# Performance work log

Measured on AMD Instinct MI355X. Metric: run time of the kernel, lower is better.

The kernel has to match this reference:

```python
import jax, jax.numpy as jnp
import numpy as np

HID, NH, NKV, HD = 2048, 16, 8, 128
EPS = 1e-6
THETA = 10000.0
SCALE = HD ** -0.5


def setup_inputs() -> dict:
    key = jax.random.key(0)
    ks = jax.random.split(key, 6)
    S = 2048
    return {
        "positions": jnp.arange(S, dtype=jnp.int32),
        "hidden_states": jax.random.normal(ks[0], (S, HID), dtype=jnp.float32),
        "layernorm_weight": jax.random.uniform(ks[1], (HID,), dtype=jnp.float32, minval=0.5, maxval=1.5),
        "w_qkv": jax.random.normal(ks[2], ((NH + 2 * NKV) * HD, HID), dtype=jnp.float32) * 0.02,
        "w_o": jax.random.normal(ks[3], (HID, NH * HD), dtype=jnp.float32) * 0.02,
        "q_norm_w": jax.random.uniform(ks[4], (HD,), dtype=jnp.float32, minval=0.5, maxval=1.5),
        "k_norm_w": jax.random.uniform(ks[5], (HD,), dtype=jnp.float32, minval=0.5, maxval=1.5),
    }


def _rmsnorm(x, w, eps=EPS):
    var = jnp.mean(jnp.square(x), axis=-1, keepdims=True)
    return x * jax.lax.rsqrt(var + eps) * w


def _rope(x, cos, sin):
    # x: [S, h, HD]; cos/sin: [S, 1, HD//2] (neox-style rotate-half)
    x1, x2 = x[..., : HD // 2], x[..., HD // 2 :]
    return jnp.concatenate([x1 * cos - x2 * sin, x2 * cos + x1 * sin], axis=-1)


def reference(positions, hidden_states, layernorm_weight, w_qkv, w_o, q_norm_w, k_norm_w):
    S = hidden_states.shape[0]
    # Fused RMSNorm + QKV projection
    hn = _rmsnorm(hidden_states, layernorm_weight)
    qkv = hn @ w_qkv.T  # [S, (NH+2*NKV)*HD]
    q, k, v = jnp.split(qkv, [NH * HD, (NH + NKV) * HD], axis=-1)
    q = q.reshape(S, NH, HD)
    k = k.reshape(S, NKV, HD)
    v = v.reshape(S, NKV, HD)
    # Per-head QK RMSNorm
    q = _rmsnorm(q, q_norm_w)
    k = _rmsnorm(k, k_norm_w)
    # RoPE
    inv_freq = 1.0 / (THETA ** (jnp.arange(0, HD, 2, dtype=jnp.float32) / HD))
    freqs = positions.astype(jnp.float32)[:, None] * inv_freq  # [S, HD//2]
    cos = jnp.cos(freqs)[:, None, :]
    sin = jnp.sin(freqs)[:, None, :]
    q = _rope(q, cos, sin)
    k = _rope(k, cos, sin)
    # GQA: expand kv heads to match query heads
    rep = NH // NKV
    k = jnp.repeat(k, rep, axis=1)  # [S, NH, HD]
    v = jnp.repeat(v, rep, axis=1)
    # Causal attention
    scores = jnp.einsum("shd,thd->hst", q, k) * SCALE  # [NH, S, S]
    causal = jnp.tril(jnp.ones((S, S), dtype=bool))
    scores = jnp.where(causal, scores, jnp.finfo(scores.dtype).min)
    probs = jax.nn.softmax(scores, axis=-1)
    out = jnp.einsum("hst,thd->shd", probs, v)  # [S, NH, HD]
    # Output projection
    return out.reshape(S, NH * HD) @ w_o.T
```

## Files before the change

kernel.cpp:

```cpp
#include <hip/hip_runtime.h>
#include <hip/hip_bf16.h>
#include <math.h>

#define HID 2048
#define NH 16
#define NKV 8
#define HD 128
#define SEQ 2048
#define EPS 1e-6f
#define SCALE 0.08838834764831845f

typedef __attribute__((ext_vector_type(8))) short bf8_t;
typedef __attribute__((ext_vector_type(4))) float f4_t;

__device__ __forceinline__ short f2bf(float f) {
    union { __hip_bfloat16 h; short s; } u;
    u.h = __float2bfloat16(f);
    return u.s;
}
__device__ __forceinline__ float bf2f(short s) {
    union { short s; __hip_bfloat16 h; } u;
    u.s = s;
    return __bfloat162float(u.h);
}
__device__ __forceinline__ bf8_t pack8(const float4& a, const float4& b) {
    bf8_t r;
    r[0] = f2bf(a.x); r[1] = f2bf(a.y); r[2] = f2bf(a.z); r[3] = f2bf(a.w);
    r[4] = f2bf(b.x); r[5] = f2bf(b.y); r[6] = f2bf(b.z); r[7] = f2bf(b.w);
    return r;
}
__device__ __forceinline__ void gload16(const short* g, short* l) {
    __builtin_amdgcn_global_load_lds(
        (const __attribute__((address_space(1))) unsigned int*)g,
        (__attribute__((address_space(3))) unsigned int*)l, 16, 0, 0);
}

__device__ __forceinline__ float wave_reduce_sum(float v) {
#pragma unroll
    for (int off = 32; off > 0; off >>= 1) v += __shfl_xor(v, off);
    return v;
}

__global__ __launch_bounds__(256) void prep_kernel(
    const float* __restrict__ w_qkv, short* __restrict__ wqb,
    const float* __restrict__ w_o, short* __restrict__ wob,
    const float* __restrict__ x, const float* __restrict__ w,
    short* __restrict__ out) {
    int bid = blockIdx.x;
    int tid = threadIdx.x;
    if (bid < 4096) {
        int i = bid * 256 + tid;
        float4 a = *(const float4*)(w_qkv + (size_t)i * 8);
        float4 b = *(const float4*)(w_qkv + (size_t)i * 8 + 4);
        *(bf8_t*)(wqb + (size_t)i * 8) = pack8(a, b);
        return;
    }
    if (bid < 6144) {
        int i = (bid - 4096) * 256 + tid;
        float4 a = *(const float4*)(w_o + (size_t)i * 8);
        float4 b = *(const float4*)(w_o + (size_t)i * 8 + 4);
        *(bf8_t*)(wob + (size_t)i * 8) = pack8(a, b);
        return;
    }
    int row = bid - 6144;
    const float* xr = x + (size_t)row * HID;
    float4 a = *(const float4*)(xr + tid * 8);
    float4 b = *(const float4*)(xr + tid * 8 + 4);
    float ss = a.x * a.x + a.y * a.y + a.z * a.z + a.w * a.w +
               b.x * b.x + b.y * b.y + b.z * b.z + b.w * b.w;
    ss = wave_reduce_sum(ss);
    __shared__ float part[4];
    __shared__ float s_scale;
    if ((tid & 63) == 0) part[tid >> 6] = ss;
    __syncthreads();
    if (tid == 0) {
        float t = part[0] + part[1] + part[2] + part[3];
        s_scale = rsqrtf(t / (float)HID + EPS);
    }
    __syncthreads();
    float sc = s_scale;
    float4 wa = *(const float4*)(w + tid * 8);
    float4 wb = *(const float4*)(w + tid * 8 + 4);
    float4 oa = make_float4(a.x * sc * wa.x, a.y * sc * wa.y,
                            a.z * sc * wa.z, a.w * sc * wa.w);
    float4 ob = make_float4(b.x * sc * wb.x, b.y * sc * wb.y,
                            b.z * sc * wb.z, b.w * sc * wb.w);
    *(bf8_t*)(out + (size_t)row * HID + tid * 8) = pack8(oa, ob);
}

template <int MODE>
__global__ __launch_bounds__(256) void gemm_mfma_kernel(
    const short* __restrict__ A, const short* __restrict__ B,
    float* __restrict__ Cf, short* __restrict__ Q, short* __restrict__ Kp,
    short* __restrict__ Vr, int M, int N, int K) {
    __shared__ short As[128][64];
    __shared__ short Bs[128][64];
    int tid = threadIdx.x;
    int wv = tid >> 6, lane = tid & 63;
    int n16 = lane & 15, qd = lane >> 4;
    int m0 = blockIdx.y * 128, n0 = blockIdx.x * 128;
    int wm = (wv >> 1) * 64, wn = (wv & 1) * 64;
    int sr8 = lane >> 3, slot = lane & 7;

    size_t ainv[4], binv[4];
#pragma unroll
    for (int it = 0; it < 4; ++it) {
        int row = wv * 32 + it * 8 + sr8;
        int chunk = (slot - row) & 7;
        ainv[it] = (size_t)(m0 + row) * K + chunk * 8;
        binv[it] = (size_t)(n0 + row) * K + chunk * 8;
    }

    f4_t acc[4][4];
#pragma unroll
    for (int i = 0; i < 4; ++i)
#pragma unroll
        for (int j = 0; j < 4; ++j) acc[i][j] = (f4_t){0.f, 0.f, 0.f, 0.f};

    for (int k0 = 0; k0 < K; k0 += 64) {
        __syncthreads();
#pragma unroll
        for (int it = 0; it < 4; ++it) {
            gload16(A + ainv[it] + k0, &As[wv * 32 + it * 8][0]);
            gload16(B + binv[it] + k0, &Bs[wv * 32 + it * 8][0]);
        }
        __syncthreads();

        bf8_t af[4][2], bf[4][2];
#pragma unroll
        for (int t = 0; t < 4; ++t)
#pragma unroll
            for (int ks = 0; ks < 2; ++ks) {
                int ar = wm + t * 16 + n16;
                af[t][ks] = *(const bf8_t*)&As[ar][(((ks * 4 + qd) + ar) & 7) * 8];
                int br = wn + t * 16 + n16;
                bf[t][ks] = *(const bf8_t*)&Bs[br][(((ks * 4 + qd) + br) & 7) * 8];
            }
#pragma unroll
        for (int ks = 0; ks < 2; ++ks)
#pragma unroll
            for (int mt = 0; mt < 4; ++mt)
#pragma unroll
                for (int nt = 0; nt < 4; ++nt)
                    acc[mt][nt] = __builtin_amdgcn_mfma_f32_16x16x32_bf16(
                        af[mt][ks], bf[nt][ks], acc[mt][nt], 0, 0, 0);
    }

#pragma unroll
    for (int mt = 0; mt < 4; ++mt)
#pragma unroll
        for (int nt = 0; nt < 4; ++nt)
#pragma unroll
            for (int r = 0; r < 4; ++r) {
                int gm = m0 + wm + mt * 16 + qd * 4 + r;
                int gn = n0 + wn + nt * 16 + n16;
                float v = acc[mt][nt][r];
                if (MODE == 0) {
                    Cf[(size_t)gm * N + gn] = v;
                } else {
                    if (gn < NH * HD)
                        Q[(size_t)gm * (NH * HD) + gn] = f2bf(v);
                    else if (gn < (NH + NKV) * HD)
                        Kp[(size_t)gm * (NKV * HD) + (gn - NH * HD)] = f2bf(v);
                    else
                        Vr[(size_t)gm * (NKV * HD) + (gn - (NH + NKV) * HD)] = f2bf(v);
                }
            }
}

__global__ __launch_bounds__(256) void mid_kernel(
    const short* __restrict__ vr, short* __restrict__ vt,
    short* __restrict__ q, short* __restrict__ k,
    const float* __restrict__ qw, const float* __restrict__ kw,
    const int* __restrict__ pos) {
    int bid = blockIdx.x;
    int tid = threadIdx.x;
    if (bid < 512) {
        __shared__ short t[64][64];
        int s0 = (bid & 31) * 64, d0 = (bid >> 5) * 64;
        int sl = tid >> 3, ch = tid & 7;
#pragma unroll
        for (int it = 0; it < 2; ++it) {
            int s_local = it * 32 + sl;
            bf8_t vv = *(const bf8_t*)(vr + (size_t)(s0 + s_local) * (NKV * HD) + d0 + ch * 8);
            *(bf8_t*)&t[s_local][((ch + s_local) & 7) * 8] = vv;
        }
        __syncthreads();
#pragma unroll
        for (int it = 0; it < 2; ++it) {
            int d_local = it * 32 + sl;
            int sbase = ch * 8;
            bf8_t o;
#pragma unroll
            for (int j = 0; j < 8; ++j) {
                int s = sbase + j;
                o[j] = t[s][(((d_local >> 3) + s) & 7) * 8 + (d_local & 7)];
            }
            *(bf8_t*)(vt + (size_t)(d0 + d_local) * SEQ + s0 + sbase) = o;
        }
        return;
    }
    int u = (bid - 512) * 2 + (tid >> 7);
    int ui = tid >> 7, d = tid & 127;
    int s = u / 24, hh = u % 24;
    short* ptr;
    const float* w;
    if (hh < NH) {
        ptr = q + (size_t)s * (NH * HD) + hh * HD;
        w = qw;
    } else {
        ptr = k + (size_t)s * (NKV * HD) + (hh - NH) * HD;
        w = kw;
    }
    float x = bf2f(ptr[d]);
    float ss = wave_reduce_sum(x * x);
    __shared__ float part[2][2];
    if ((d & 63) == 0) part[ui][d >> 6] = ss;
    __syncthreads();
    float tot = part[ui][0] + part[ui][1];
    float xn = x * rsqrtf(tot / (float)HD + EPS) * w[d];
    __shared__ float sh[2][HD];
    sh[ui][d] = xn;
    __syncthreads();
    int j = d & 63;
    float inv = powf(10000.0f, -(float)(2 * j) * (1.0f / (float)HD));
    float fr = (float)pos[s] * inv;
    float sn, cs;
    sincosf(fr, &sn, &cs);
    float o;
    if (d < 64)
        o = xn * cs - sh[ui][d + 64] * sn;
    else
        o = xn * cs + sh[ui][d - 64] * sn;
    ptr[d] = f2bf(o);
}

__device__ __forceinline__ void attn_stage(
    short (&kb)[64][128], short (&vb)[128][64],
    const short* __restrict__ kg, const short* __restrict__ vg,
    int t0, const int (&kinv)[4], const int (&vinv)[4], int wv) {
#pragma unroll
    for (int it = 0; it < 4; ++it) {
        gload16(kg + (size_t)t0 * (NKV * HD) + kinv[it], &kb[wv * 16 + it * 4][0]);
        gload16(vg + t0 + vinv[it], &vb[wv * 32 + it * 8][0]);
    }
}

__device__ __forceinline__ void attn_tile(
    const short (&kb)[64][128], const short (&vb)[128][64],
    short (&psh)[4][16][72],
    const bf8_t (&qf)[4], f4_t (&of)[8],
    float (&m_i)[4], float (&l_p)[4],
    int wv, int n, int qd, bool diag) {
    f4_t sc[4];
#pragma unroll
    for (int kk = 0; kk < 4; ++kk) sc[kk] = (f4_t){0.f, 0.f, 0.f, 0.f};
#pragma unroll
    for (int kk = 0; kk < 4; ++kk) {
        int key = kk * 16 + n;
#pragma unroll
        for (int ks = 0; ks < 4; ++ks) {
            bf8_t kf = *(const bf8_t*)&kb[key][(((ks * 4 + qd) + key) & 15) * 8];
            sc[kk] = __builtin_amdgcn_mfma_f32_16x16x32_bf16(qf[ks], kf, sc[kk], 0, 0, 0);
        }
    }
    int rowb = wv * 16 + qd * 4;
#pragma unroll
    for (int kk = 0; kk < 4; ++kk)
#pragma unroll
        for (int r = 0; r < 4; ++r) {
            float s = sc[kk][r] * SCALE;
            if (diag && (kk * 16 + n > rowb + r)) s = -1e30f;
            sc[kk][r] = s;
        }
#pragma unroll
    for (int r = 0; r < 4; ++r) {
        float mx = fmaxf(fmaxf(sc[0][r], sc[1][r]), fmaxf(sc[2][r], sc[3][r]));
#pragma unroll
        for (int off = 1; off < 16; off <<= 1) mx = fmaxf(mx, __shfl_xor(mx, off));
        float mnew = fmaxf(m_i[r], mx);
        float al = __expf(m_i[r] - mnew);
        m_i[r] = mnew;
        float lsum = 0.f;
#pragma unroll
        for (int kk = 0; kk < 4; ++kk) {
            float p = __expf(sc[kk][r] - mnew);
            psh[wv][qd * 4 + r][kk * 16 + n] = f2bf(p);
            lsum += p;
        }
        l_p[r] = l_p[r] * al + lsum;
#pragma unroll
        for (int nb = 0; nb < 8; ++nb) of[nb][r] *= al;
    }
    __builtin_amdgcn_wave_barrier();
#pragma unroll
    for (int ks2 = 0; ks2 < 2; ++ks2) {
        bf8_t pf = *(const bf8_t*)&psh[wv][n][ks2 * 32 + qd * 8];
#pragma unroll
        for (int nb = 0; nb < 8; ++nb) {
            int dim = nb * 16 + n;
            bf8_t vf = *(const bf8_t*)&vb[dim][(((ks2 * 4 + qd) + dim) & 7) * 8];
            of[nb] = __builtin_amdgcn_mfma_f32_16x16x32_bf16(pf, vf, of[nb], 0, 0, 0);
        }
    }
}

__global__ __launch_bounds__(256) void attn_chunk_kernel(
    const short* __restrict__ q, const short* __restrict__ k,
    const short* __restrict__ vt, short* __restrict__ o,
    short* __restrict__ opart, float* __restrict__ ml) {
    __shared__ short kbufA[64][128], kbufB[64][128];
    __shared__ short vbufA[128][64], vbufB[128][64];
    __shared__ short psh[4][16][72];

    int tid = threadIdx.x;
    int wv = tid >> 6, lane = tid & 63;
    int n = lane & 15, qd = lane >> 4;

    int bid = blockIdx.x;
    int h, qb, tstart, tcount, c;
    bool split;
    if (bid < 512) {
        int id = bid;
        qb = 16 + (id >> 5);
        c = (id >> 4) & 1;
        h = id & 15;
        if (c == 0) { tstart = 0; tcount = 16; }
        else        { tstart = 16; tcount = qb - 15; }
        split = true;
    } else {
        int id = bid - 512;
        qb = 15 - (id >> 4);
        h = id & 15;
        tstart = 0; tcount = qb + 1; c = 0;
        split = false;
    }
    bool dl = (tstart + tcount - 1 == qb);
    int kvh = h >> 1;
    int qbase = qb * 64;

    int kinv[4], vinv[4];
#pragma unroll
    for (int it = 0; it < 4; ++it) {
        int key = wv * 16 + it * 4 + (lane >> 4);
        int ck = ((lane & 15) - key) & 15;
        kinv[it] = key * (NKV * HD) + kvh * HD + ck * 8;
        int dim = wv * 32 + it * 8 + (lane >> 3);
        int cv = ((lane & 7) - dim) & 7;
        vinv[it] = (kvh * HD + dim) * SEQ + cv * 8;
    }

    bf8_t qf[4];
    {
        const short* qp = q + (size_t)(qbase + wv * 16 + n) * (NH * HD) + h * HD + qd * 8;
#pragma unroll
        for (int ks = 0; ks < 4; ++ks) qf[ks] = *(const bf8_t*)(qp + ks * 32);
    }

    f4_t of[8];
#pragma unroll
    for (int i = 0; i < 8; ++i) of[i] = (f4_t){0.f, 0.f, 0.f, 0.f};
    float m_i[4] = {-1e30f, -1e30f, -1e30f, -1e30f};
    float l_p[4] = {0.f, 0.f, 0.f, 0.f};

    attn_stage(kbufA, vbufA, k, vt, tstart * 64, kinv, vinv, wv);
    for (int tt = 0; tt < tcount; tt += 2) {
        __syncthreads();
        if (tt + 1 < tcount)
            attn_stage(kbufB, vbufB, k, vt, (tstart + tt + 1) * 64, kinv, vinv, wv);
        attn_tile(kbufA, vbufA, psh, qf, of, m_i, l_p, wv, n, qd, dl && (tt == tcount - 1));
        if (tt + 1 < tcount) {
            __syncthreads();
            if (tt + 2 < tcount)
                attn_stage(kbufA, vbufA, k, vt, (tstart + tt + 2) * 64, kinv, vinv, wv);
            attn_tile(kbufB, vbufB, psh, qf, of, m_i, l_p, wv, n, qd, dl && (tt + 1 == tcount - 1));
        }
    }

    float lred[4];
#pragma unroll
    for (int r = 0; r < 4; ++r) {
        float l = l_p[r];
#pragma unroll
        for (int off = 1; off < 16; off <<= 1) l += __shfl_xor(l, off);
        lred[r] = l;
    }

    if (!split) {
#pragma unroll
        for (int nb = 0; nb < 8; ++nb)
#pragma unroll
            for (int r = 0; r < 4; ++r) {
                int row = qbase + wv * 16 + qd * 4 + r;
                o[(size_t)row * (NH * HD) + h * HD + nb * 16 + n] =
                    f2bf(of[nb][r] / lred[r]);
            }
    } else {
        size_t pb = ((size_t)h * 16 + (qb - 16)) * 2 + c;
        short* op = opart + pb * (64 * 128);
#pragma unroll
        for (int nb = 0; nb < 8; ++nb)
#pragma unroll
            for (int r = 0; r < 4; ++r) {
                int rl = wv * 16 + qd * 4 + r;
                op[rl * 128 + nb * 16 + n] = f2bf(of[nb][r]);
            }
        if (n == 0) {
#pragma unroll
            for (int r = 0; r < 4; ++r) {
                int rl = wv * 16 + qd * 4 + r;
                ml[pb * 128 + rl * 2] = m_i[r];
                ml[pb * 128 + rl * 2 + 1] = lred[r];
            }
        }
    }
}

__global__ __launch_bounds__(256) void attn_merge_kernel(
    const short* __restrict__ opart, const float* __restrict__ ml,
    short* __restrict__ o) {
    int bid = blockIdx.x;
    int h = bid & 15, qi = bid >> 4;
    int tid = threadIdx.x;
    int r = tid >> 2, dq = tid & 3;
    size_t pb0 = ((size_t)h * 16 + qi) * 2;
    size_t pb1 = pb0 + 1;
    float m0 = ml[pb0 * 128 + r * 2], l0 = ml[pb0 * 128 + r * 2 + 1];
    float m1 = ml[pb1 * 128 + r * 2], l1 = ml[pb1 * 128 + r * 2 + 1];
    float M = fmaxf(m0, m1);
    float w0 = __expf(m0 - M), w1 = __expf(m1 - M);
    float invL = 1.0f / (w0 * l0 + w1 * l1);
    int row = (16 + qi) * 64 + r;
#pragma unroll
    for (int j = 0; j < 4; ++j) {
        int d0 = dq * 32 + j * 8;
        bf8_t a = *(const bf8_t*)(opart + pb0 * (64 * 128) + r * 128 + d0);
        bf8_t b = *(const bf8_t*)(opart + pb1 * (64 * 128) + r * 128 + d0);
        bf8_t e;
#pragma unroll
        for (int i = 0; i < 8; ++i)
            e[i] = f2bf((w0 * bf2f(a[i]) + w1 * bf2f(b[i])) * invL);
        *(bf8_t*)(o + (size_t)row * (NH * HD) + h * HD + d0) = e;
    }
}

extern "C" void kernel_launch(void* const* d_in, const int* in_sizes, int n_in,
                              void* d_out, int out_size, void* d_ws, size_t ws_size,
                              hipStream_t stream) {
    const int* positions   = (const int*)d_in[0];
    const float* hidden    = (const float*)d_in[1];
    const float* ln_w      = (const float*)d_in[2];
    const float* w_qkv     = (const float*)d_in[3];
    const float* w_o       = (const float*)d_in[4];
    const float* q_norm_w  = (const float*)d_in[5];
    const float* k_norm_w  = (const float*)d_in[6];
    float* out = (float*)d_out;

    char* base = (char*)d_ws;
    short* hnb   = (short*)(base);
    short* wqb   = (short*)(base + ((size_t)8 << 20));
    short* vtb   = (short*)(base + ((size_t)8 << 20));
    short* opart = (short*)(base + ((size_t)12 << 20));
    float* mlbuf = (float*)(base + ((size_t)20 << 20));
    short* wob   = (short*)(base + ((size_t)24 << 20));
    short* qbf   = (short*)(base + ((size_t)32 << 20));
    short* kbf   = (short*)(base + ((size_t)40 << 20));
    short* vrow  = (short*)(base + ((size_t)44 << 20));

    prep_kernel<<<8192, 256, 0, stream>>>(w_qkv, wqb, w_o, wob, hidden, ln_w, hnb);
    gemm_mfma_kernel<1><<<dim3(32, 16), 256, 0, stream>>>(
        hnb, wqb, nullptr, qbf, kbf, vrow, SEQ, (NH + 2 * NKV) * HD, HID);
    mid_kernel<<<512 + 24576, 256, 0, stream>>>(
        vrow, vtb, qbf, kbf, q_norm_w, k_norm_w, positions);
    attn_chunk_kernel<<<768, 256, 0, stream>>>(qbf, kbf, vtb, hnb, opart, mlbuf);
    attn_merge_kernel<<<256, 256, 0, stream>>>(opart, mlbuf, hnb);
    gemm_mfma_kernel<0><<<dim3(16, 16), 256, 0, stream>>>(
        hnb, wob, out, nullptr, nullptr, nullptr, SEQ, NH * HD, HID);
}
```

Baseline: 300.8 us.

## Process 128-row query tiles per block with balanced causal split and merge

Each attention block now handles 128 query rows (two 16-row groups per wave), so every K/V tile loaded to LDS is reused by twice as many queries. Work is split into 512 blocks that pair a short and a long causal range per query tile, and every tile goes through the merge kernel. The partial outputs are staged in the output buffer. Other changes: an XOR-swizzled P buffer, launch_bounds of 2, and fast exp/sincos in the RoPE step. The costs are higher register pressure, a merge pass that now covers all rows, and lower precision in the RoPE angle math.

```diff
diff --git a/kernel.cpp b/kernel.cpp
--- a/kernel.cpp
+++ b/kernel.cpp
@@ -223,10 +223,10 @@
     sh[ui][d] = xn;
     __syncthreads();
     int j = d & 63;
-    float inv = powf(10000.0f, -(float)(2 * j) * (1.0f / (float)HD));
+    float inv = __expf((float)j * -0.14391156831f);
     float fr = (float)pos[s] * inv;
     float sn, cs;
-    sincosf(fr, &sn, &cs);
+    __sincosf(fr, &sn, &cs);
     float o;
     if (d < 64)
         o = xn * cs - sh[ui][d + 64] * sn;
@@ -248,96 +248,95 @@
 
 __device__ __forceinline__ void attn_tile(
     const short (&kb)[64][128], const short (&vb)[128][64],
-    short (&psh)[4][16][72],
-    const bf8_t (&qf)[4], f4_t (&of)[8],
-    float (&m_i)[4], float (&l_p)[4],
-    int wv, int n, int qd, bool diag) {
-    f4_t sc[4];
-#pragma unroll
-    for (int kk = 0; kk < 4; ++kk) sc[kk] = (f4_t){0.f, 0.f, 0.f, 0.f};
+    short (&psh)[4][2][16][64],
+    const bf8_t (&qf)[2][4], f4_t (&of)[2][8],
+    float (&m_i)[2][4], float (&l_p)[2][4],
+    int wv, int n, int qd, int koff) {
+    f4_t sc[2][4];
+#pragma unroll
+    for (int g = 0; g < 2; ++g)
+#pragma unroll
+        for (int kk = 0; kk < 4; ++kk) sc[g][kk] = (f4_t){0.f, 0.f, 0.f, 0.f};
 #pragma unroll
     for (int kk = 0; kk < 4; ++kk) {
         int key = kk * 16 + n;
 #pragma unroll
         for (int ks = 0; ks < 4; ++ks) {
             bf8_t kf = *(const bf8_t*)&kb[key][(((ks * 4 + qd) + key) & 15) * 8];
-            sc[kk] = __builtin_amdgcn_mfma_f32_16x16x32_bf16(qf[ks], kf, sc[kk], 0, 0, 0);
-        }
-    }
-    int rowb = wv * 16 + qd * 4;
-#pragma unroll
-    for (int kk = 0; kk < 4; ++kk)
+            sc[0][kk] = __builtin_amdgcn_mfma_f32_16x16x32_bf16(qf[0][ks], kf, sc[0][kk], 0, 0, 0);
+            sc[1][kk] = __builtin_amdgcn_mfma_f32_16x16x32_bf16(qf[1][ks], kf, sc[1][kk], 0, 0, 0);
+        }
+    }
+#pragma unroll
+    for (int g = 0; g < 2; ++g) {
+        int rows0 = wv * 32 + g * 16;
+        bool needm = (koff + 63 > rows0);
+#pragma unroll
+        for (int kk = 0; kk < 4; ++kk)
+#pragma unroll
+            for (int r = 0; r < 4; ++r) {
+                float s = sc[g][kk][r] * SCALE;
+                if (needm && (koff + kk * 16 + n > rows0 + qd * 4 + r)) s = -1e30f;
+                sc[g][kk][r] = s;
+            }
 #pragma unroll
         for (int r = 0; r < 4; ++r) {
-            float s = sc[kk][r] * SCALE;
-            if (diag && (kk * 16 + n > rowb + r)) s = -1e30f;
-            sc[kk][r] = s;
-        }
-#pragma unroll
-    for (int r = 0; r < 4; ++r) {
-        float mx = fmaxf(fmaxf(sc[0][r], sc[1][r]), fmaxf(sc[2][r], sc[3][r]));
-#pragma unroll
-        for (int off = 1; off < 16; off <<= 1) mx = fmaxf(mx, __shfl_xor(mx, off));
-        float mnew = fmaxf(m_i[r], mx);
-        float al = __expf(m_i[r] - mnew);
-        m_i[r] = mnew;
-        float lsum = 0.f;
-#pragma unroll
-        for (int kk = 0; kk < 4; ++kk) {
-            float p = __expf(sc[kk][r] - mnew);
-            psh[wv][qd * 4 + r][kk * 16 + n] = f2bf(p);
-            lsum += p;
-        }
-        l_p[r] = l_p[r] * al + lsum;
-#pragma unroll
-        for (int nb = 0; nb < 8; ++nb) of[nb][r] *= al;
+            float mx = fmaxf(fmaxf(sc[g][0][r], sc[g][1][r]),
+                             fmaxf(sc[g][2][r], sc[g][3][r]));
+#pragma unroll
+            for (int off = 1; off < 16; off <<= 1) mx = fmaxf(mx, __shfl_xor(mx, off));
+            float mnew = fmaxf(m_i[g][r], mx);
+            float al = __expf(m_i[g][r] - mnew);
+            m_i[g][r] = mnew;
+            float lsum = 0.f;
+            int row = qd * 4 + r;
+#pragma unroll
+            for (int kk = 0; kk < 4; ++kk) {
+                float p = __expf(sc[g][kk][r] - mnew);
+                psh[wv][g][row][((kk * 16 + n) + row * 8) & 63] = f2bf(p);
+                lsum += p;
+            }
+            l_p[g][r] = l_p[g][r] * al + lsum;
+#pragma unroll
+            for (int nb = 0; nb < 8; ++nb) of[g][nb][r] *= al;
+        }
     }
     __builtin_amdgcn_wave_barrier();
 #pragma unroll
     for (int ks2 = 0; ks2 < 2; ++ks2) {
-        bf8_t pf = *(const bf8_t*)&psh[wv][n][ks2 * 32 + qd * 8];
+        bf8_t pf0 = *(const bf8_t*)&psh[wv][0][n][((ks2 * 32 + qd * 8) + n * 8) & 63];
+        bf8_t pf1 = *(const bf8_t*)&psh[wv][1][n][((ks2 * 32 + qd * 8) + n * 8) & 63];
 #pragma unroll
         for (int nb = 0; nb < 8; ++nb) {
             int dim = nb * 16 + n;
             bf8_t vf = *(const bf8_t*)&vb[dim][(((ks2 * 4 + qd) + dim) & 7) * 8];
-            of[nb] = __builtin_amdgcn_mfma_f32_16x16x32_bf16(pf, vf, of[nb], 0, 0, 0);
-        }
-    }
-}
-
-__global__ __launch_bounds__(256) void attn_chunk_kernel(
+            of[0][nb] = __builtin_amdgcn_mfma_f32_16x16x32_bf16(pf0, vf, of[0][nb], 0, 0, 0);
+            of[1][nb] = __builtin_amdgcn_mfma_f32_16x16x32_bf16(pf1, vf, of[1][nb], 0, 0, 0);
+        }
+    }
+}
+
+__global__ __launch_bounds__(256, 2) void attn_chunk_kernel(
     const short* __restrict__ q, const short* __restrict__ k,
-    const short* __restrict__ vt, short* __restrict__ o,
-    short* __restrict__ opart, float* __restrict__ ml) {
+    const short* __restrict__ vt, short* __restrict__ opart,
+    float* __restrict__ ml) {
     __shared__ short kbufA[64][128], kbufB[64][128];
     __shared__ short vbufA[128][64], vbufB[128][64];
-    __shared__ short psh[4][16][72];
+    __shared__ short psh[4][2][16][64];
 
     int tid = threadIdx.x;
     int wv = tid >> 6, lane = tid & 63;
     int n = lane & 15, qd = lane >> 4;
 
-    int bid = blockIdx.x;
-    int h, qb, tstart, tcount, c;
-    bool split;
-    if (bid < 512) {
-        int id = bid;
-        qb = 16 + (id >> 5);
-        c = (id >> 4) & 1;
-        h = id & 15;
-        if (c == 0) { tstart = 0; tcount = 16; }
-        else        { tstart = 16; tcount = qb - 15; }
-        split = true;
-    } else {
-        int id = bid - 512;
-        qb = 15 - (id >> 4);
-        h = id & 15;
-        tstart = 0; tcount = qb + 1; c = 0;
-        split = false;
-    }
-    bool dl = (tstart + tcount - 1 == qb);
+    int i = blockIdx.x;
+    int hs = i >> 8, p = i & 255;
+    int h = p >> 4;
+    int qt = hs ? (p & 15) : (15 - (p & 15));
+    int c = hs;
+    int qbase = qt * 128;
+    int tstart = c ? (qt + 1) : 0;
+    int tcount = qt + 1;
     int kvh = h >> 1;
-    int qbase = qb * 64;
 
     int kinv[4], vinv[4];
 #pragma unroll
@@ -350,69 +349,71 @@
         vinv[it] = (kvh * HD + dim) * SEQ + cv * 8;
     }
 
-    bf8_t qf[4];
-    {
-        const short* qp = q + (size_t)(qbase + wv * 16 + n) * (NH * HD) + h * HD + qd * 8;
-#pragma unroll
-        for (int ks = 0; ks < 4; ++ks) qf[ks] = *(const bf8_t*)(qp + ks * 32);
-    }
-
-    f4_t of[8];
-#pragma unroll
-    for (int i = 0; i < 8; ++i) of[i] = (f4_t){0.f, 0.f, 0.f, 0.f};
-    float m_i[4] = {-1e30f, -1e30f, -1e30f, -1e30f};
-    float l_p[4] = {0.f, 0.f, 0.f, 0.f};
+    bf8_t qf[2][4];
+#pragma unroll
+    for (int g = 0; g < 2; ++g) {
+        const short* qp =
+            q + (size_t)(qbase + wv * 32 + g * 16 + n) * (NH * HD) + h * HD + qd * 8;
+#pragma unroll
+        for (int ks = 0; ks < 4; ++ks) qf[g][ks] = *(const bf8_t*)(qp + ks * 32);
+    }
+
+    f4_t of[2][8];
+#pragma unroll
+    for (int g = 0; g < 2; ++g)
+#pragma unroll
+        for (int x = 0; x < 8; ++x) of[g][x] = (f4_t){0.f, 0.f, 0.f, 0.f};
+    float m_i[2][4] = {{-1e30f, -1e30f, -1e30f, -1e30f},
+                       {-1e30f, -1e30f, -1e30f, -1e30f}};
+    float l_p[2][4] = {{0.f, 0.f, 0.f, 0.f}, {0.f, 0.f, 0.f, 0.f}};
 
     attn_stage(kbufA, vbufA, k, vt, tstart * 64, kinv, vinv, wv);
     for (int tt = 0; tt < tcount; tt += 2) {
         __syncthreads();
         if (tt + 1 < tcount)
             attn_stage(kbufB, vbufB, k, vt, (tstart + tt + 1) * 64, kinv, vinv, wv);
-        attn_tile(kbufA, vbufA, psh, qf, of, m_i, l_p, wv, n, qd, dl && (tt == tcount - 1));
+        attn_tile(kbufA, vbufA, psh, qf, of, m_i, l_p, wv, n, qd,
+                  (tstart + tt) * 64 - qbase);
         if (tt + 1 < tcount) {
             __syncthreads();
             if (tt + 2 < tcount)
                 attn_stage(kbufA, vbufA, k, vt, (tstart + tt + 2) * 64, kinv, vinv, wv);
-            attn_tile(kbufB, vbufB, psh, qf, of, m_i, l_p, wv, n, qd, dl && (tt + 1 == tcount - 1));
-        }
-    }
-
-    float lred[4];
-#pragma unroll
-    for (int r = 0; r < 4; ++r) {
-        float l = l_p[r];
-#pragma unroll
-        for (int off = 1; off < 16; off <<= 1) l += __shfl_xor(l, off);
-        lred[r] = l;
-    }
-
-    if (!split) {
+            attn_tile(kbufB, vbufB, psh, qf, of, m_i, l_p, wv, n, qd,
+                      (tstart + tt + 1) * 64 - qbase);
+        }
+    }
+
+    float lred[2][4];
+#pragma unroll
+    for (int g = 0; g < 2; ++g)
+#pragma unroll
+        for (int r = 0; r < 4; ++r) {
+            float l = l_p[g][r];
+#pragma unroll
+            for (int off = 1; off < 16; off <<= 1) l += __shfl_xor(l, off);
+            lred[g][r] = l;
+        }
+
+    size_t pb = ((size_t)(h * 16 + qt)) * 2 + c;
+    short* op = opart + pb * (128 * 128);
+#pragma unroll
+    for (int g = 0; g < 2; ++g)
 #pragma unroll
         for (int nb = 0; nb < 8; ++nb)
 #pragma unroll
             for (int r = 0; r < 4; ++r) {
-                int row = qbase + wv * 16 + qd * 4 + r;
-                o[(size_t)row * (NH * HD) + h * HD + nb * 16 + n] =
-                    f2bf(of[nb][r] / lred[r]);
-            }
-    } else {
-        size_t pb = ((size_t)h * 16 + (qb - 16)) * 2 + c;
-        short* op = opart + pb * (64 * 128);
-#pragma unroll
-        for (int nb = 0; nb < 8; ++nb)
+                int rl = wv * 32 + g * 16 + qd * 4 + r;
+                op[rl * 128 + nb * 16 + n] = f2bf(of[g][nb][r]);
+            }
+    if (n == 0) {
+#pragma unroll
+        for (int g = 0; g < 2; ++g)
 #pragma unroll
             for (int r = 0; r < 4; ++r) {
-                int rl = wv * 16 + qd * 4 + r;
-                op[rl * 128 + nb * 16 + n] = f2bf(of[nb][r]);
-            }
-        if (n == 0) {
-#pragma unroll
-            for (int r = 0; r < 4; ++r) {
-                int rl = wv * 16 + qd * 4 + r;
-                ml[pb * 128 + rl * 2] = m_i[r];
-                ml[pb * 128 + rl * 2 + 1] = lred[r];
-            }
-        }
+                int rl = wv * 32 + g * 16 + qd * 4 + r;
+                ml[pb * 256 + rl * 2] = m_i[g][r];
+                ml[pb * 256 + rl * 2 + 1] = lred[g][r];
+            }
     }
 }
 
@@ -420,26 +421,26 @@
     const short* __restrict__ opart, const float* __restrict__ ml,
     short* __restrict__ o) {
     int bid = blockIdx.x;
-    int h = bid & 15, qi = bid >> 4;
+    int h = bid >> 4, qt = bid & 15;
     int tid = threadIdx.x;
-    int r = tid >> 2, dq = tid & 3;
-    size_t pb0 = ((size_t)h * 16 + qi) * 2;
+    int r = tid >> 1, hf = tid & 1;
+    size_t pb0 = ((size_t)(h * 16 + qt)) * 2;
     size_t pb1 = pb0 + 1;
-    float m0 = ml[pb0 * 128 + r * 2], l0 = ml[pb0 * 128 + r * 2 + 1];
-    float m1 = ml[pb1 * 128 + r * 2], l1 = ml[pb1 * 128 + r * 2 + 1];
+    float m0 = ml[pb0 * 256 + r * 2], l0 = ml[pb0 * 256 + r * 2 + 1];
+    float m1 = ml[pb1 * 256 + r * 2], l1 = ml[pb1 * 256 + r * 2 + 1];
     float M = fmaxf(m0, m1);
     float w0 = __expf(m0 - M), w1 = __expf(m1 - M);
     float invL = 1.0f / (w0 * l0 + w1 * l1);
-    int row = (16 + qi) * 64 + r;
-#pragma unroll
-    for (int j = 0; j < 4; ++j) {
-        int d0 = dq * 32 + j * 8;
-        bf8_t a = *(const bf8_t*)(opart + pb0 * (64 * 128) + r * 128 + d0);
-        bf8_t b = *(const bf8_t*)(opart + pb1 * (64 * 128) + r * 128 + d0);
+    int row = qt * 128 + r;
+#pragma unroll
+    for (int j = 0; j < 8; ++j) {
+        int d0 = hf * 64 + j * 8;
+        bf8_t a = *(const bf8_t*)(opart + pb0 * (128 * 128) + r * 128 + d0);
+        bf8_t b = *(const bf8_t*)(opart + pb1 * (128 * 128) + r * 128 + d0);
         bf8_t e;
 #pragma unroll
-        for (int i = 0; i < 8; ++i)
-            e[i] = f2bf((w0 * bf2f(a[i]) + w1 * bf2f(b[i])) * invL);
+        for (int x = 0; x < 8; ++x)
+            e[x] = f2bf((w0 * bf2f(a[x]) + w1 * bf2f(b[x])) * invL);
         *(bf8_t*)(o + (size_t)row * (NH * HD) + h * HD + d0) = e;
     }
 }
@@ -460,19 +461,19 @@
     short* hnb   = (short*)(base);
     short* wqb   = (short*)(base + ((size_t)8 << 20));
     short* vtb   = (short*)(base + ((size_t)8 << 20));
-    short* opart = (short*)(base + ((size_t)12 << 20));
-    float* mlbuf = (float*)(base + ((size_t)20 << 20));
+    float* mlbuf = (float*)(base + ((size_t)12 << 20));
     short* wob   = (short*)(base + ((size_t)24 << 20));
     short* qbf   = (short*)(base + ((size_t)32 << 20));
     short* kbf   = (short*)(base + ((size_t)40 << 20));
     short* vrow  = (short*)(base + ((size_t)44 << 20));
+    short* opart = (short*)d_out;
 
     prep_kernel<<<8192, 256, 0, stream>>>(w_qkv, wqb, w_o, wob, hidden, ln_w, hnb);
     gemm_mfma_kernel<1><<<dim3(32, 16), 256, 0, stream>>>(
         hnb, wqb, nullptr, qbf, kbf, vrow, SEQ, (NH + 2 * NKV) * HD, HID);
     mid_kernel<<<512 + 24576, 256, 0, stream>>>(
         vrow, vtb, qbf, kbf, q_norm_w, k_norm_w, positions);
-    attn_chunk_kernel<<<768, 256, 0, stream>>>(qbf, kbf, vtb, hnb, opart, mlbuf);
+    attn_chunk_kernel<<<512, 256, 0, stream>>>(qbf, kbf, vtb, opart, mlbuf);
     attn_merge_kernel<<<256, 256, 0, stream>>>(opart, mlbuf, hnb);
     gemm_mfma_kernel<0><<<dim3(16, 16), 256, 0, stream>>>(
         hnb, wob, out, nullptr, nullptr, nullptr, SEQ, NH * HD, HID);
```

New measurement: 279.3 us. -7.1%, faster.
